# Optimization experiments

Hardware: AMD Instinct MI355X
Metric: run time of the kernel (lower is better)

Reference implementation:

```python
import jax, jax.numpy as jnp
import numpy as np

D_MODEL = 1024
NUM_HEADS = 16
D_K = D_MODEL // NUM_HEADS
MAX_SEQ_LEN = 2048
THETA = 10000.0


def rotation_matrix_table(theta, d_k, max_seq_len):
    # [max_seq_len, d_k, d_k] block-diagonal 2x2 rotation matrices,
    # same math as the torch reference's generate_rotation_matrix.
    pos = jnp.arange(max_seq_len, dtype=jnp.float32)            # [S]
    kidx = jnp.arange(d_k // 2, dtype=jnp.float32)              # [d_k/2]
    angles = pos[:, None] / (theta ** (2.0 * kidx / d_k))       # [S, d_k/2]
    cos, sin = jnp.cos(angles), jnp.sin(angles)
    rot = jnp.zeros((max_seq_len, d_k, d_k), dtype=jnp.float32)
    ev = jnp.arange(0, d_k, 2)
    od = ev + 1
    rot = rot.at[:, ev, ev].set(cos)
    rot = rot.at[:, ev, od].set(-sin)
    rot = rot.at[:, od, ev].set(sin)
    rot = rot.at[:, od, od].set(cos)
    return rot


def setup_inputs() -> dict:
    key = jax.random.key(0)
    k0, k1, k2, k3, k4 = jax.random.split(key, 5)
    B, S = 4, 2048
    std = np.sqrt(2.0 / (D_MODEL + D_MODEL))
    return {
        "in_features": jax.random.normal(k0, (B, S, D_MODEL), dtype=jnp.float32),
        "wq": jax.random.normal(k1, (D_MODEL, D_MODEL), dtype=jnp.float32) * std,
        "wk": jax.random.normal(k2, (D_MODEL, D_MODEL), dtype=jnp.float32) * std,
        "wv": jax.random.normal(k3, (D_MODEL, D_MODEL), dtype=jnp.float32) * std,
        "wo": jax.random.normal(k4, (D_MODEL, D_MODEL), dtype=jnp.float32) * std,
    }


def reference(in_features, wq, wk, wv, wo):
    B, S, _ = in_features.shape
    H, Dk = NUM_HEADS, D_K
    # QKV projections (weights stored [out, in], applied as x @ W.T)
    q = in_features @ wq.T
    k = in_features @ wk.T
    v = in_features @ wv.T
    # [B, H, S, Dk]
    q = q.reshape(B, S, H, Dk).transpose(0, 2, 1, 3)
    k = k.reshape(B, S, H, Dk).transpose(0, 2, 1, 3)
    v = v.reshape(B, S, H, Dk).transpose(0, 2, 1, 3)
    # RoPE via dense per-position rotation matrix (faithful to source)
    rot = rotation_matrix_table(THETA, Dk, MAX_SEQ_LEN)[:S]     # [S, Dk, Dk]
    q = jnp.einsum("sde,bhse->bhsd", rot, q)
    k = jnp.einsum("sde,bhse->bhsd", rot, k)
    # scaled dot-product attention with causal mask
    scores = jnp.einsum("bhqd,bhkd->bhqk", q, k) / np.sqrt(Dk)
    causal = jnp.tril(jnp.ones((S, S), dtype=bool))             # True = keep
    scores = jnp.where(causal[None, None], scores, -jnp.inf)
    attn = jax.nn.softmax(scores, axis=-1)
    out = jnp.einsum("bhqk,bhkd->bhqd", attn, v)
    out = out.transpose(0, 2, 1, 3).reshape(B, S, H * Dk)
    return out @ wo.T
```

## Files before the change

kernel.cpp:

```cpp
#include <hip/hip_runtime.h>

#define SEQ     2048
#define DMODEL  1024
#define NHEADS  16
#define DKH     64
#define BATCH   4

typedef __bf16 bf16x8 __attribute__((ext_vector_type(8)));
typedef float  f32x4  __attribute__((ext_vector_type(4)));
typedef float  f32x16 __attribute__((ext_vector_type(16)));

static __device__ __forceinline__ unsigned short f2bf(float x) {
  unsigned int u = __float_as_uint(x);
  u += 0x7fffu + ((u >> 16) & 1u);
  return (unsigned short)(u >> 16);
}
static __device__ __forceinline__ float bf2f(unsigned short b) {
  return __uint_as_float(((unsigned int)b) << 16);
}
static __device__ __forceinline__ void gload_lds16(const void* g, void* lds) {
  __builtin_amdgcn_global_load_lds((const __attribute__((address_space(1))) void*)g,
                                   (__attribute__((address_space(3))) void*)lds,
                                   16, 0, 0);
}
static __device__ __forceinline__ f32x4 mfma16(bf16x8 a, bf16x8 b, f32x4 c) {
  return __builtin_amdgcn_mfma_f32_16x16x32_bf16(a, b, c, 0, 0, 0);
}
static __device__ __forceinline__ f32x16 mfma32(bf16x8 a, bf16x8 b, f32x16 c) {
  return __builtin_amdgcn_mfma_f32_32x32x16_bf16(a, b, c, 0, 0, 0);
}

__global__ void cast_kernel(const float* __restrict__ src,
                            unsigned short* __restrict__ dst, int n4) {
  int i = blockIdx.x * 256 + threadIdx.x;
  if (i >= n4) return;
  float4 v = ((const float4*)src)[i];
  ushort4 o;
  o.x = f2bf(v.x); o.y = f2bf(v.y); o.z = f2bf(v.z); o.w = f2bf(v.w);
  ((ushort4*)dst)[i] = o;
}

__global__ void cast4_kernel(const float* __restrict__ s0, const float* __restrict__ s1,
                             const float* __restrict__ s2, const float* __restrict__ s3,
                             unsigned short* __restrict__ d0, unsigned short* __restrict__ d1,
                             unsigned short* __restrict__ d2, unsigned short* __restrict__ d3,
                             int n4) {
  int i = blockIdx.x * 256 + threadIdx.x;
  if (i >= n4) return;
  const float* s = (blockIdx.y == 0) ? s0 : (blockIdx.y == 1) ? s1 : (blockIdx.y == 2) ? s2 : s3;
  unsigned short* d = (blockIdx.y == 0) ? d0 : (blockIdx.y == 1) ? d1 : (blockIdx.y == 2) ? d2 : d3;
  float4 v = ((const float4*)s)[i];
  ushort4 o;
  o.x = f2bf(v.x); o.y = f2bf(v.y); o.z = f2bf(v.z); o.w = f2bf(v.w);
  ((ushort4*)d)[i] = o;
}

template<int EPI>
__global__ __launch_bounds__(256)
void gemm_bt(const unsigned short* __restrict__ A,
             const unsigned short* __restrict__ W0,
             const unsigned short* __restrict__ W1,
             const unsigned short* __restrict__ W2,
             unsigned short* __restrict__ O0,
             unsigned short* __restrict__ O1,
             unsigned short* __restrict__ O2,
             float* __restrict__ Of)
{
  __shared__ unsigned short smem[4][128*64];
  const int tid = threadIdx.x;
  const int lane = tid & 63, w = tid >> 6;
  const int wm = w >> 1, wn = w & 1;
  const int l31 = lane & 31, lg2 = lane >> 5;

  const int NWG = (EPI == 0) ? 1536 : 512;
  const int CPX = NWG / 8;
  const int lgid = (blockIdx.x & 7) * CPX + (blockIdx.x >> 3);
  const int n0 = (lgid & 7) * 128;
  const int m0 = ((lgid >> 3) & 63) * 128;
  const int z  = (EPI == 0) ? (lgid >> 9) : 0;
  const unsigned short* Bw = (EPI == 0)
      ? ((z == 0) ? W0 : ((z == 1) ? W1 : W2)) : W0;

  f32x16 acc[2][2];
  #pragma unroll
  for (int a = 0; a < 2; ++a)
    #pragma unroll
    for (int b = 0; b < 2; ++b)
      #pragma unroll
      for (int r = 0; r < 16; ++r)
        acc[a][b][r] = 0.f;

  auto STAGE = [&](int buf, int t) {
    const int k0 = t * 64;
    #pragma unroll
    for (int it = 0; it < 4; ++it) {
      int c = it*4 + w;
      int off16 = c*64 + lane;
      int r = off16 >> 3, p = off16 & 7;
      int s = p ^ (r & 7);
      gload_lds16(A  + (size_t)(m0 + r)*DMODEL + k0 + s*8, (char*)smem[buf]     + c*1024);
      gload_lds16(Bw + (size_t)(n0 + r)*DMODEL + k0 + s*8, (char*)smem[2 + buf] + c*1024);
    }
  };

  const int NT = DMODEL / 64;
  STAGE(0, 0);
  STAGE(1, 1);

  for (int t = 0; t < NT; ++t) {
    const int cur = t & 1;
    if (t == NT - 1) asm volatile("s_waitcnt vmcnt(0)" ::: "memory");
    else             asm volatile("s_waitcnt vmcnt(8)" ::: "memory");
    __builtin_amdgcn_s_barrier();
    __builtin_amdgcn_sched_barrier(0);

    #pragma unroll
    for (int ks = 0; ks < 4; ++ks) {
      bf16x8 af[2], bg[2];
      #pragma unroll
      for (int bi = 0; bi < 2; ++bi) {
        int row = wm*64 + bi*32 + l31;
        int sp = (ks*2 + lg2) ^ (row & 7);
        af[bi] = *(const bf16x8*)((const char*)smem[cur] + row*128 + sp*16);
      }
      #pragma unroll
      for (int bj = 0; bj < 2; ++bj) {
        int row = wn*64 + bj*32 + l31;
        int sp = (ks*2 + lg2) ^ (row & 7);
        bg[bj] = *(const bf16x8*)((const char*)smem[2 + cur] + row*128 + sp*16);
      }
      __builtin_amdgcn_s_setprio(1);
      #pragma unroll
      for (int bi = 0; bi < 2; ++bi)
        #pragma unroll
        for (int bj = 0; bj < 2; ++bj)
          acc[bi][bj] = mfma32(af[bi], bg[bj], acc[bi][bj]);
      __builtin_amdgcn_s_setprio(0);
    }

    __builtin_amdgcn_sched_barrier(0);
    __builtin_amdgcn_s_barrier();
    __builtin_amdgcn_sched_barrier(0);
    if (t + 2 < NT) STAGE(cur, t + 2);
  }

  if (EPI == 1) {
    #pragma unroll
    for (int bi = 0; bi < 2; ++bi)
      #pragma unroll
      for (int bj = 0; bj < 2; ++bj)
        #pragma unroll
        for (int r = 0; r < 16; ++r) {
          int m = m0 + wm*64 + bi*32 + (r & 3) + 8*(r >> 2) + 4*lg2;
          int n = n0 + wn*64 + bj*32 + l31;
          Of[(size_t)m*DMODEL + n] = acc[bi][bj][r];
        }
    return;
  }

  unsigned short* Odst = (z == 0) ? O0 : ((z == 1) ? O1 : O2);

  if (z == 2) {
    unsigned short* tb = (unsigned short*)smem;
    #pragma unroll
    for (int bi = 0; bi < 2; ++bi)
      #pragma unroll
      for (int bj = 0; bj < 2; ++bj) {
        int n_loc = wn*64 + bj*32 + l31;
        #pragma unroll
        for (int g = 0; g < 4; ++g) {
          int m_loc = wm*64 + bi*32 + 8*g + 4*lg2;
          ushort4 pk;
          pk.x = f2bf(acc[bi][bj][g*4 + 0]);
          pk.y = f2bf(acc[bi][bj][g*4 + 1]);
          pk.z = f2bf(acc[bi][bj][g*4 + 2]);
          pk.w = f2bf(acc[bi][bj][g*4 + 3]);
          *(ushort4*)(tb + n_loc*136 + m_loc) = pk;
        }
      }
    __syncthreads();
    const int bb  = m0 >> 11;
    const int sq0 = m0 & (SEQ - 1);
    const size_t obase = (size_t)bb * NHEADS * DKH * SEQ;
    #pragma unroll
    for (int it = 0; it < 8; ++it) {
      int nn = it*16 + (tid >> 4);
      int cc = tid & 15;
      bf16x8 v8 = *(const bf16x8*)(tb + nn*136 + cc*8);
      int hh = (n0 + nn) >> 6;
      int dk = nn & 63;
      *(bf16x8*)&Odst[obase + ((size_t)hh*DKH + dk)*SEQ + sq0 + cc*8] = v8;
    }
  } else {
    float invf2[2];
    #pragma unroll
    for (int bj = 0; bj < 2; ++bj)
      invf2[bj] = exp2f(-0.41524101186092029f * (float)((bj*32 + l31) >> 1));
    #pragma unroll
    for (int bi = 0; bi < 2; ++bi)
      #pragma unroll
      for (int bj = 0; bj < 2; ++bj)
        #pragma unroll
        for (int r = 0; r < 16; ++r) {
          int m = m0 + wm*64 + bi*32 + (r & 3) + 8*(r >> 2) + 4*lg2;
          int n = n0 + wn*64 + bj*32 + l31;
          float v = acc[bi][bj][r];
          int b = m >> 11, sq = m & (SEQ-1), hh = n >> 6, dk = n & 63;
          float prt = __shfl_xor(v, 1);
          float ang = (float)sq * invf2[bj];
          float sn, cs;
          __sincosf(ang, &sn, &cs);
          float out = (l31 & 1) ? (sn*prt + cs*v) : (cs*v - sn*prt);
          if (z == 0) out *= 0.18033688011112043f;
          Odst[(((size_t)b*NHEADS + hh)*SEQ + sq)*DKH + dk] = f2bf(out);
        }
  }
}

__global__ __launch_bounds__(512)
void attn_kernel(const unsigned short* __restrict__ Qg,
                 const unsigned short* __restrict__ Kg,
                 const unsigned short* __restrict__ Vtg,
                 unsigned short* __restrict__ Og)
{
  const int lgid = (blockIdx.x & 7) * 64 + (blockIdx.x >> 3);
  const int px = lgid & 7;
  const int bh = lgid >> 3;
  const int tid = threadIdx.x;
  const int lane = tid & 63, w = tid >> 6;
  const int li = lane & 15, lg = lane >> 4;
  const float THRL2 = 11.0f;

  __shared__ unsigned short sK[2][64*64];
  __shared__ unsigned short sV[2][64*64];
  __shared__ unsigned short sP[8][16*72];
  unsigned short* sPw = sP[w];

  const size_t bhBase = (size_t)bh * SEQ * DKH;

  bf16x8 onesf;
  {
    __bf16 ob = (__bf16)1.0f;
    #pragma unroll
    for (int j = 0; j < 8; ++j) onesf[j] = ob;
  }
  const f32x4 fz = {0.f, 0.f, 0.f, 0.f};

  auto STAGE = [&](int buf, int t) {
    const int kv0 = t * 64;
    int off16 = w*64 + lane;
    int r = off16 >> 3, p = off16 & 7;
    int s = p ^ (r & 7);
    gload_lds16(Kg  + bhBase + (size_t)(kv0 + r)*DKH + s*8, (char*)sK[buf] + w*1024);
    gload_lds16(Vtg + bhBase + (size_t)r*SEQ + kv0 + s*8,   (char*)sV[buf] + w*1024);
  };

  #pragma unroll 1
  for (int pass = 0; pass < 2; ++pass) {
    const int qt = pass ? (15 - px) : px;
    const int q0 = qt * 128;
    const int myrow0 = q0 + w*16;

    bf16x8 qf[2];
    {
      const unsigned short* qp = Qg + bhBase + (size_t)(myrow0 + li)*DKH + lg*8;
      qf[0] = *(const bf16x8*)qp;
      qf[1] = *(const bf16x8*)(qp + 32);
    }

    f32x4 acc_o[4], ls4;
    float m_r[4];
    #pragma unroll
    for (int nt = 0; nt < 4; ++nt) acc_o[nt] = fz;
    ls4 = fz;
    #pragma unroll
    for (int kr = 0; kr < 4; ++kr) m_r[kr] = -1e30f;

    const int nt_stage = 2*qt + 2;
    const int last_t  = 2*qt + (w >= 4 ? 1 : 0);

    STAGE(0, 0);
    STAGE(1, 1);

    for (int t = 0; t < nt_stage; ++t) {
      const int cur = t & 1;
      if (t == nt_stage - 1) asm volatile("s_waitcnt vmcnt(0)" ::: "memory");
      else                   asm volatile("s_waitcnt vmcnt(2)" ::: "memory");
      __builtin_amdgcn_s_barrier();
      __builtin_amdgcn_sched_barrier(0);

      if (t <= last_t) {
        const int kv0 = t * 64;
        f32x4 sc[4];
        #pragma unroll
        for (int nt = 0; nt < 4; ++nt) sc[nt] = fz;
        __builtin_amdgcn_s_setprio(1);
        #pragma unroll
        for (int kf = 0; kf < 2; ++kf) {
          #pragma unroll
          for (int nt = 0; nt < 4; ++nt) {
            int row = nt*16 + li;
            int sp = (kf*4 + lg) ^ (row & 7);
            bf16x8 kb = *(const bf16x8*)(sK[cur] + row*64 + sp*8);
            sc[nt] = mfma16(qf[kf], kb, sc[nt]);
          }
        }
        __builtin_amdgcn_s_setprio(0);

        if (t == last_t) {
          #pragma unroll
          for (int nt = 0; nt < 4; ++nt)
            #pragma unroll
            for (int kr = 0; kr < 4; ++kr) {
              int col = kv0 + nt*16 + li;
              int row = myrow0 + lg*4 + kr;
              if (col > row) sc[nt][kr] = -1e30f;
            }
        }

        float pm[4];
        #pragma unroll
        for (int kr = 0; kr < 4; ++kr)
          pm[kr] = fmaxf(fmaxf(sc[0][kr], sc[1][kr]), fmaxf(sc[2][kr], sc[3][kr]));
        int need = (pm[0] > m_r[0] + THRL2) | (pm[1] > m_r[1] + THRL2) |
                   (pm[2] > m_r[2] + THRL2) | (pm[3] > m_r[3] + THRL2);
        if (__any(need)) {
          #pragma unroll
          for (int kr = 0; kr < 4; ++kr) {
            float m2 = pm[kr];
            m2 = fmaxf(m2, __shfl_xor(m2, 1));
            m2 = fmaxf(m2, __shfl_xor(m2, 2));
            m2 = fmaxf(m2, __shfl_xor(m2, 4));
            m2 = fmaxf(m2, __shfl_xor(m2, 8));
            float mn = fmaxf(m_r[kr], m2);
            float scl = __builtin_amdgcn_exp2f(m_r[kr] - mn);
            m_r[kr] = mn;
            #pragma unroll
            for (int nt = 0; nt < 4; ++nt) acc_o[nt][kr] *= scl;
            ls4[kr] *= scl;
          }
        }
        #pragma unroll
        for (int nt = 0; nt < 4; ++nt)
          #pragma unroll
          for (int kr = 0; kr < 4; ++kr)
            sc[nt][kr] = __builtin_amdgcn_exp2f(sc[nt][kr] - m_r[kr]);

        #pragma unroll
        for (int nt = 0; nt < 4; ++nt)
          #pragma unroll
          for (int kr = 0; kr < 4; ++kr)
            sPw[(lg*4 + kr)*72 + nt*16 + li] = f2bf(sc[nt][kr]);

        bf16x8 pa[2];
        #pragma unroll
        for (int kf = 0; kf < 2; ++kf)
          pa[kf] = *(const bf16x8*)(sPw + li*72 + kf*32 + lg*8);

        __builtin_amdgcn_s_setprio(1);
        ls4 = mfma16(pa[0], onesf, ls4);
        ls4 = mfma16(pa[1], onesf, ls4);
        #pragma unroll
        for (int kf = 0; kf < 2; ++kf)
          #pragma unroll
          for (int nt = 0; nt < 4; ++nt) {
            int rr = nt*16 + li;
            int sp = (kf*4 + lg) ^ (rr & 7);
            bf16x8 vb = *(const bf16x8*)(sV[cur] + rr*64 + sp*8);
            acc_o[nt] = mfma16(pa[kf], vb, acc_o[nt]);
          }
        __builtin_amdgcn_s_setprio(0);
      }

      __builtin_amdgcn_sched_barrier(0);
      __builtin_amdgcn_s_barrier();
      __builtin_amdgcn_sched_barrier(0);
      if (t + 2 < nt_stage) STAGE(cur, t + 2);
    }

    const int b = bh >> 4, hh = bh & 15;
    #pragma unroll
    for (int kr = 0; kr < 4; ++kr) {
      float inv = __builtin_amdgcn_rcpf(ls4[kr]);
      int srow = myrow0 + lg*4 + kr;
      size_t orow = ((size_t)b*SEQ + srow)*DMODEL + (size_t)hh*DKH;
      #pragma unroll
      for (int nt = 0; nt < 4; ++nt)
        Og[orow + nt*16 + li] = f2bf(acc_o[nt][kr] * inv);
    }
  }
}

extern "C" void kernel_launch(void* const* d_in, const int* in_sizes, int n_in,
                              void* d_out, int out_size, void* d_ws, size_t ws_size,
                              hipStream_t stream)
{
  (void)in_sizes; (void)n_in; (void)out_size; (void)ws_size;
  const float* X  = (const float*)d_in[0];
  const float* Wq = (const float*)d_in[1];
  const float* Wk = (const float*)d_in[2];
  const float* Wv = (const float*)d_in[3];
  const float* Wo = (const float*)d_in[4];

  char* ws = (char*)d_ws;
  const size_t SZ_X = (size_t)8192 * 1024 * 2;
  const size_t SZ_W = (size_t)1024 * 1024 * 2;
  unsigned short* Xb  = (unsigned short*)(ws);
  unsigned short* Wqb = (unsigned short*)(ws + SZ_X);
  unsigned short* Wkb = (unsigned short*)(ws + SZ_X + 1*SZ_W);
  unsigned short* Wvb = (unsigned short*)(ws + SZ_X + 2*SZ_W);
  unsigned short* Wob = (unsigned short*)(ws + SZ_X + 3*SZ_W);
  unsigned short* Vtb = (unsigned short*)(ws + SZ_X + 4*SZ_W);
  unsigned short* Qb  = (unsigned short*)d_out;
  unsigned short* Kb  = Qb + (size_t)8192 * 1024;
  unsigned short* Ob  = Xb;

  cast_kernel<<<8192, 256, 0, stream>>>(X, Xb, 8388608/4);
  cast4_kernel<<<dim3(1024, 4), 256, 0, stream>>>(Wq, Wk, Wv, Wo,
                                                  Wqb, Wkb, Wvb, Wob, 1048576/4);

  gemm_bt<0><<<1536, 256, 0, stream>>>(Xb, Wqb, Wkb, Wvb, Qb, Kb, Vtb, nullptr);
  attn_kernel<<<512, 512, 0, stream>>>(Qb, Kb, Vtb, Ob);
  gemm_bt<1><<<512, 256, 0, stream>>>(Ob, Wob, nullptr, nullptr,
                                      nullptr, nullptr, nullptr,
                                      (float*)d_out);
}
```

Measured before the change: 169.6 us.

## Compute transposed scores and pass P through register shuffles instead of LDS

The QK^T MFMA operands are swapped so each lane holds scores for one query row across 16 key positions. The per-row max and sum then need only two cross-lane shuffles, and the ones-vector MFMA used for the row sum is gone. P is packed to bf16 with v_cvt_pk_bf16_f32 and permuted into the A-operand layout with ds_bpermute-style shuffles, removing the per-wave LDS scratch write/read round trip. In exchange it adds many shuffles per tile and extra shuffles to broadcast the rescale factors and row sums.

```diff
diff --git a/kernel.cpp b/kernel.cpp
--- a/kernel.cpp
+++ b/kernel.cpp
@@ -28,6 +28,17 @@
 }
 static __device__ __forceinline__ f32x16 mfma32(bf16x8 a, bf16x8 b, f32x16 c) {
   return __builtin_amdgcn_mfma_f32_32x32x16_bf16(a, b, c, 0, 0, 0);
+}
+static __device__ __forceinline__ unsigned cvtpk_bf16(float lo, float hi) {
+  unsigned r;
+  asm("v_cvt_pk_bf16_f32 %0, %1, %2" : "=v"(r) : "v"(lo), "v"(hi));
+  return r;
+}
+static __device__ __forceinline__ bf16x8 pack4(unsigned a, unsigned b,
+                                               unsigned c, unsigned d) {
+  union { unsigned u[4]; bf16x8 v; } t;
+  t.u[0] = a; t.u[1] = b; t.u[2] = c; t.u[3] = d;
+  return t.v;
 }
 
 __global__ void cast_kernel(const float* __restrict__ src,
@@ -233,17 +244,8 @@
 
   __shared__ unsigned short sK[2][64*64];
   __shared__ unsigned short sV[2][64*64];
-  __shared__ unsigned short sP[8][16*72];
-  unsigned short* sPw = sP[w];
 
   const size_t bhBase = (size_t)bh * SEQ * DKH;
-
-  bf16x8 onesf;
-  {
-    __bf16 ob = (__bf16)1.0f;
-    #pragma unroll
-    for (int j = 0; j < 8; ++j) onesf[j] = ob;
-  }
   const f32x4 fz = {0.f, 0.f, 0.f, 0.f};
 
   auto STAGE = [&](int buf, int t) {
@@ -255,26 +257,29 @@
     gload_lds16(Vtg + bhBase + (size_t)r*SEQ + kv0 + s*8,   (char*)sV[buf] + w*1024);
   };
 
+  const int srcA = li + (((2*lg)     & 3) << 4);
+  const int srcB = li + (((2*lg + 1) & 3) << 4);
+  const bool hi2 = (lg >= 2);
+
   #pragma unroll 1
   for (int pass = 0; pass < 2; ++pass) {
     const int qt = pass ? (15 - px) : px;
     const int q0 = qt * 128;
     const int myrow0 = q0 + w*16;
+    const int qrow = myrow0 + li;
 
     bf16x8 qf[2];
     {
-      const unsigned short* qp = Qg + bhBase + (size_t)(myrow0 + li)*DKH + lg*8;
+      const unsigned short* qp = Qg + bhBase + (size_t)qrow*DKH + lg*8;
       qf[0] = *(const bf16x8*)qp;
       qf[1] = *(const bf16x8*)(qp + 32);
     }
 
-    f32x4 acc_o[4], ls4;
-    float m_r[4];
+    f32x4 acc_o[4];
     #pragma unroll
     for (int nt = 0; nt < 4; ++nt) acc_o[nt] = fz;
-    ls4 = fz;
-    #pragma unroll
-    for (int kr = 0; kr < 4; ++kr) m_r[kr] = -1e30f;
+    float m_r = -1e30f;
+    float ls  = 0.f;
 
     const int nt_stage = 2*qt + 2;
     const int last_t  = 2*qt + (w >= 4 ? 1 : 0);
@@ -302,7 +307,7 @@
             int row = nt*16 + li;
             int sp = (kf*4 + lg) ^ (row & 7);
             bf16x8 kb = *(const bf16x8*)(sK[cur] + row*64 + sp*8);
-            sc[nt] = mfma16(qf[kf], kb, sc[nt]);
+            sc[nt] = mfma16(kb, qf[kf], sc[nt]);
           }
         }
         __builtin_amdgcn_s_setprio(0);
@@ -312,63 +317,86 @@
           for (int nt = 0; nt < 4; ++nt)
             #pragma unroll
             for (int kr = 0; kr < 4; ++kr) {
-              int col = kv0 + nt*16 + li;
-              int row = myrow0 + lg*4 + kr;
-              if (col > row) sc[nt][kr] = -1e30f;
+              int kv = kv0 + nt*16 + lg*4 + kr;
+              if (kv > qrow) sc[nt][kr] = -1e30f;
             }
         }
 
-        float pm[4];
-        #pragma unroll
-        for (int kr = 0; kr < 4; ++kr)
-          pm[kr] = fmaxf(fmaxf(sc[0][kr], sc[1][kr]), fmaxf(sc[2][kr], sc[3][kr]));
-        int need = (pm[0] > m_r[0] + THRL2) | (pm[1] > m_r[1] + THRL2) |
-                   (pm[2] > m_r[2] + THRL2) | (pm[3] > m_r[3] + THRL2);
-        if (__any(need)) {
+        float pm = sc[0][0];
+        #pragma unroll
+        for (int nt = 0; nt < 4; ++nt)
+          #pragma unroll
+          for (int kr = 0; kr < 4; ++kr)
+            pm = fmaxf(pm, sc[nt][kr]);
+        if (__any(pm > m_r + THRL2)) {
+          float m2 = pm;
+          m2 = fmaxf(m2, __shfl_xor(m2, 16));
+          m2 = fmaxf(m2, __shfl_xor(m2, 32));
+          float mn = fmaxf(m_r, m2);
+          float scl = __builtin_amdgcn_exp2f(m_r - mn);
+          m_r = mn;
+          ls *= scl;
+          float sclk[4];
+          #pragma unroll
+          for (int kr = 0; kr < 4; ++kr)
+            sclk[kr] = __shfl(scl, lg*4 + kr);
+          #pragma unroll
+          for (int nt = 0; nt < 4; ++nt)
+            #pragma unroll
+            for (int kr = 0; kr < 4; ++kr)
+              acc_o[nt][kr] *= sclk[kr];
+        }
+
+        float rs = 0.f;
+        #pragma unroll
+        for (int nt = 0; nt < 4; ++nt)
           #pragma unroll
           for (int kr = 0; kr < 4; ++kr) {
-            float m2 = pm[kr];
-            m2 = fmaxf(m2, __shfl_xor(m2, 1));
-            m2 = fmaxf(m2, __shfl_xor(m2, 2));
-            m2 = fmaxf(m2, __shfl_xor(m2, 4));
-            m2 = fmaxf(m2, __shfl_xor(m2, 8));
-            float mn = fmaxf(m_r[kr], m2);
-            float scl = __builtin_amdgcn_exp2f(m_r[kr] - mn);
-            m_r[kr] = mn;
-            #pragma unroll
-            for (int nt = 0; nt < 4; ++nt) acc_o[nt][kr] *= scl;
-            ls4[kr] *= scl;
+            float pv = __builtin_amdgcn_exp2f(sc[nt][kr] - m_r);
+            sc[nt][kr] = pv;
+            rs += pv;
           }
-        }
-        #pragma unroll
-        for (int nt = 0; nt < 4; ++nt)
-          #pragma unroll
-          for (int kr = 0; kr < 4; ++kr)
-            sc[nt][kr] = __builtin_amdgcn_exp2f(sc[nt][kr] - m_r[kr]);
-
-        #pragma unroll
-        for (int nt = 0; nt < 4; ++nt)
-          #pragma unroll
-          for (int kr = 0; kr < 4; ++kr)
-            sPw[(lg*4 + kr)*72 + nt*16 + li] = f2bf(sc[nt][kr]);
-
-        bf16x8 pa[2];
-        #pragma unroll
-        for (int kf = 0; kf < 2; ++kf)
-          pa[kf] = *(const bf16x8*)(sPw + li*72 + kf*32 + lg*8);
+        rs += __shfl_xor(rs, 16);
+        rs += __shfl_xor(rs, 32);
+        ls += rs;
+
+        unsigned u00 = cvtpk_bf16(sc[0][0], sc[0][1]);
+        unsigned u01 = cvtpk_bf16(sc[0][2], sc[0][3]);
+        unsigned u10 = cvtpk_bf16(sc[1][0], sc[1][1]);
+        unsigned u11 = cvtpk_bf16(sc[1][2], sc[1][3]);
+        unsigned u20 = cvtpk_bf16(sc[2][0], sc[2][1]);
+        unsigned u21 = cvtpk_bf16(sc[2][2], sc[2][3]);
+        unsigned u30 = cvtpk_bf16(sc[3][0], sc[3][1]);
+        unsigned u31 = cvtpk_bf16(sc[3][2], sc[3][3]);
+
+        unsigned a00 = __shfl(u00, srcA), a10 = __shfl(u10, srcA);
+        unsigned a01 = __shfl(u01, srcA), a11 = __shfl(u11, srcA);
+        unsigned b00 = __shfl(u00, srcB), b10 = __shfl(u10, srcB);
+        unsigned b01 = __shfl(u01, srcB), b11 = __shfl(u11, srcB);
+        bf16x8 pa0 = pack4(hi2 ? a10 : a00, hi2 ? a11 : a01,
+                           hi2 ? b10 : b00, hi2 ? b11 : b01);
+        unsigned c20 = __shfl(u20, srcA), c30 = __shfl(u30, srcA);
+        unsigned c21 = __shfl(u21, srcA), c31 = __shfl(u31, srcA);
+        unsigned d20 = __shfl(u20, srcB), d30 = __shfl(u30, srcB);
+        unsigned d21 = __shfl(u21, srcB), d31 = __shfl(u31, srcB);
+        bf16x8 pa1 = pack4(hi2 ? c30 : c20, hi2 ? c31 : c21,
+                           hi2 ? d30 : d20, hi2 ? d31 : d21);
 
         __builtin_amdgcn_s_setprio(1);
-        ls4 = mfma16(pa[0], onesf, ls4);
-        ls4 = mfma16(pa[1], onesf, ls4);
-        #pragma unroll
-        for (int kf = 0; kf < 2; ++kf)
-          #pragma unroll
-          for (int nt = 0; nt < 4; ++nt) {
-            int rr = nt*16 + li;
-            int sp = (kf*4 + lg) ^ (rr & 7);
-            bf16x8 vb = *(const bf16x8*)(sV[cur] + rr*64 + sp*8);
-            acc_o[nt] = mfma16(pa[kf], vb, acc_o[nt]);
-          }
+        #pragma unroll
+        for (int nt = 0; nt < 4; ++nt) {
+          int rr = nt*16 + li;
+          int sp0 = (0*4 + lg) ^ (rr & 7);
+          bf16x8 vb0 = *(const bf16x8*)(sV[cur] + rr*64 + sp0*8);
+          acc_o[nt] = mfma16(pa0, vb0, acc_o[nt]);
+        }
+        #pragma unroll
+        for (int nt = 0; nt < 4; ++nt) {
+          int rr = nt*16 + li;
+          int sp1 = (1*4 + lg) ^ (rr & 7);
+          bf16x8 vb1 = *(const bf16x8*)(sV[cur] + rr*64 + sp1*8);
+          acc_o[nt] = mfma16(pa1, vb1, acc_o[nt]);
+        }
         __builtin_amdgcn_s_setprio(0);
       }
 
@@ -381,7 +409,8 @@
     const int b = bh >> 4, hh = bh & 15;
     #pragma unroll
     for (int kr = 0; kr < 4; ++kr) {
-      float inv = __builtin_amdgcn_rcpf(ls4[kr]);
+      float lsr = __shfl(ls, lg*4 + kr);
+      float inv = __builtin_amdgcn_rcpf(lsr);
       int srow = myrow0 + lg*4 + kr;
       size_t orow = ((size_t)b*SEQ + srow)*DMODEL + (size_t)hh*DKH;
       #pragma unroll
```

After: 176.0 us. 3.8% more time.
